# Performance work log

Measured on AMD Instinct MI355X. Metric: run time of the kernel, lower is better.

The kernel has to match this reference:

```python
import jax, jax.numpy as jnp
import numpy as np

B, N, T, D = 64, 76, 128, 128
AH, HEADS, DFF, FAH = 8, 4, 512, 128
DK = D // HEADS


def layer_norm(x, a, b, eps=1e-7):
    mean = x.mean(-1, keepdims=True)
    std = jnp.std(x, -1, ddof=1, keepdims=True)  # torch.std is unbiased
    return a * (x - mean) / (std + eps) + b


def setup_inputs() -> dict:
    key = jax.random.key(0)
    ks = jax.random.split(key, 32)
    w = lambda i, shape, s=0.05: (jax.random.normal(ks[i], shape, jnp.float32) * s)
    return {
        "H": jax.random.normal(ks[0], (B, N, T, D), jnp.float32),
        "mask": jax.random.randint(ks[1], (B, N, T), 0, 2).astype(jnp.float32),
        "feature_mask": jax.random.uniform(ks[2], (B, N), dtype=jnp.float32),
        # MissingAwareTemporalAttention params (shared across features)
        "Wt": w(3, (D, AH), 0.1), "Wx": w(4, (D, AH), 0.1),
        "rate": jnp.array([0.8], jnp.float32),
        "obs_bias": jnp.float32(0.5), "miss_bias": jnp.float32(0.0),
        # MultiHeadedAttention params (weights stored [in,out])
        "Wq": w(5, (D, D)), "bq": jnp.zeros(D, jnp.float32),
        "Wk": w(6, (D, D)), "bk": jnp.zeros(D, jnp.float32),
        "Wv": w(7, (D, D)), "bv": jnp.zeros(D, jnp.float32),
        "Wo": w(8, (D, D)), "bo": jnp.zeros(D, jnp.float32),
        # SublayerConnection LayerNorms
        "ln1_a": jnp.ones(D, jnp.float32), "ln1_b": jnp.zeros(D, jnp.float32),
        "ln2_a": jnp.ones(D, jnp.float32), "ln2_b": jnp.zeros(D, jnp.float32),
        # PositionwiseFeedForward
        "w1": w(9, (D, DFF)), "b1": jnp.zeros(DFF, jnp.float32),
        "w2": w(10, (DFF, D)), "b2": jnp.zeros(D, jnp.float32),
        # FinalAttentionQKV ('mul')
        "fWq": w(11, (D, FAH)), "fbq": jnp.zeros(FAH, jnp.float32),
        "fWk": w(12, (D, FAH)), "fbk": jnp.zeros(FAH, jnp.float32),
        "fWv": w(13, (D, FAH)), "fbv": jnp.zeros(FAH, jnp.float32),
        "mask_scale": jnp.float32(1.0),
    }


def concare_forward(H, mask, feature_mask, Wt, Wx, rate, obs_bias, miss_bias,
                    Wq, bq, Wk, bk, Wv, bv, Wo, bo, ln1_a, ln1_b, ln2_a, ln2_b,
                    w1, b1, w2, b2, fWq, fbq, fWk, fbk, fWv, fbv, mask_scale):
    # ---- MissingAwareTemporalAttention per feature (vectorized over N) ----
    q = jnp.einsum('bnd,da->bna', H[:, :, -1, :], Wt)           # [B,N,AH]
    k = jnp.einsum('bntd,da->bnta', H, Wx)                      # [B,N,T,AH]
    dot = jnp.einsum('bna,bnta->bnt', q, k)                     # [B,N,T]
    b_time = (jnp.arange(T - 1, -1, -1, dtype=jnp.float32) + 1.0)  # [T]
    sig = jax.nn.sigmoid(dot)
    denom = jax.nn.sigmoid(rate[0]) * (jnp.log(2.72 + (1.0 - sig)) * b_time)
    e = jax.nn.relu(sig / denom)
    e = e + jnp.where(mask > 0.5, obs_bias, miss_bias)
    a = jax.nn.softmax(e, axis=-1)                              # over T
    emb = jnp.einsum('bnt,bntd->bnd', a, H)                     # [B,N,D]

    # ---- SublayerConnection 1: pre-norm + MultiHeadedAttention + residual ----
    x0 = layer_norm(emb, ln1_a, ln1_b)
    qh = (x0 @ Wq + bq).reshape(B, N, HEADS, DK).transpose(0, 2, 1, 3)
    kh = (x0 @ Wk + bk).reshape(B, N, HEADS, DK).transpose(0, 2, 1, 3)
    vh = (x0 @ Wv + bv).reshape(B, N, HEADS, DK).transpose(0, 2, 1, 3)
    scores = jnp.einsum('bhqd,bhkd->bhqk', qh, kh) / np.sqrt(DK)
    p = jax.nn.softmax(scores, axis=-1)
    ctx = jnp.einsum('bhqk,bhkd->bhqd', p, vh).transpose(0, 2, 1, 3).reshape(B, N, D)
    mha = ctx @ Wo + bo                                          # [B,N,D]
    # DeCov regularizer over batch, per feature position
    feats = jnp.transpose(mha, (1, 2, 0))                        # [N,D,B]
    centered = feats - feats.mean(axis=2, keepdims=True)
    cov = jnp.einsum('ndb,neb->nde', centered, centered) / (B - 1)
    diag = jnp.einsum('ndd->nd', cov)
    decov = 0.5 * (jnp.sum(cov ** 2) - jnp.sum(diag ** 2))
    x = emb + mha

    # ---- SublayerConnection 2: pre-norm + FFN + residual ----
    x1 = layer_norm(x, ln2_a, ln2_b)
    ffn = jax.nn.relu(x1 @ w1 + b1) @ w2 + b2
    x = x + ffn                                                  # [B,N,D]

    # ---- FinalAttentionQKV ('mul') ----
    fq = x[:, -1, :] @ fWq + fbq                                 # [B,FAH]
    fk = x @ fWk + fbk                                           # [B,N,FAH]
    fv = x @ fWv + fbv                                           # [B,N,FAH]
    fe = jnp.einsum('bna,ba->bn', fk, fq)
    fe = fe + mask_scale * feature_mask
    alpha = jax.nn.softmax(fe, axis=1)                           # over N
    pooled = jnp.einsum('bn,bna->ba', alpha, fv)                 # [B,FAH]
    return pooled, decov


def reference(H, mask, feature_mask, Wt, Wx, rate, obs_bias, miss_bias,
              Wq, bq, Wk, bk, Wv, bv, Wo, bo, ln1_a, ln1_b, ln2_a, ln2_b,
              w1, b1, w2, b2, fWq, fbq, fWk, fbk, fWv, fbv, mask_scale):
    return concare_forward(H, mask, feature_mask, Wt, Wx, rate, obs_bias, miss_bias,
                           Wq, bq, Wk, bk, Wv, bv, Wo, bo, ln1_a, ln1_b, ln2_a, ln2_b,
                           w1, b1, w2, b2, fWq, fbq, fWk, fbk, fWv, fbv, mask_scale)
```

## Files before the change

kernel.cpp:

```cpp
#include <hip/hip_runtime.h>
#include <hip/hip_bf16.h>
#include <math.h>

#define BB 64
#define NN 76
#define TT 128
#define DD 128
#define AH 8
#define NHEADS 4
#define DFF 512
#define FAH 128
#define DK 32
#define BN (BB*NN)
#define ROWS 8
#define NBLK (BN/ROWS)

__global__ __launch_bounds__(512, 6) void k1_temporal(
    const float* __restrict__ H, const float* __restrict__ mask,
    const float* __restrict__ Wt, const float* __restrict__ Wx,
    const float* __restrict__ rate, const float* __restrict__ obs_bias,
    const float* __restrict__ miss_bias, float* __restrict__ emb)
{
    __shared__ __align__(16) float wqs[DD];
    __shared__ __align__(16) float dots[TT];
    __shared__ __align__(16) float as_[TT];
    __shared__ __align__(16) float parts[16][DD];
    __shared__ float qpart[2][AH];
    __shared__ float redmax[2];
    __shared__ float redsum[2];

    const int bid = blockIdx.x;
    const int tid = threadIdx.x;
    const size_t base = (size_t)bid * (TT*DD);

    float r127 = 0.f, maskv = 0.f;
    float4 wt0, wt1, wx0, wx1;
    if (tid < DD) {
        r127 = H[base + (TT-1)*DD + tid];
        wt0 = *(const float4*)&Wt[tid*AH + 0];
        wt1 = *(const float4*)&Wt[tid*AH + 4];
        wx0 = *(const float4*)&Wx[tid*AH + 0];
        wx1 = *(const float4*)&Wx[tid*AH + 4];
        maskv = mask[(size_t)bid*TT + tid];
    }
    const float ratev = rate[0], obsv = obs_bias[0], missv = miss_bias[0];

    float4 h[8];
    const float4* Hg4 = (const float4*)(H + base);
    #pragma unroll
    for (int j = 0; j < 8; ++j) h[j] = Hg4[j*512 + tid];

    if (tid < DD) {
        float p[AH] = {r127*wt0.x, r127*wt0.y, r127*wt0.z, r127*wt0.w,
                       r127*wt1.x, r127*wt1.y, r127*wt1.z, r127*wt1.w};
        #pragma unroll
        for (int a = 0; a < AH; ++a) {
            float v = p[a];
            #pragma unroll
            for (int m = 1; m < 64; m <<= 1) v += __shfl_xor(v, m, 64);
            if ((tid & 63) == 0) qpart[tid >> 6][a] = v;
        }
    }
    __syncthreads();
    if (tid < DD) {
        const float q0 = qpart[0][0]+qpart[1][0], q1 = qpart[0][1]+qpart[1][1];
        const float q2 = qpart[0][2]+qpart[1][2], q3 = qpart[0][3]+qpart[1][3];
        const float q4 = qpart[0][4]+qpart[1][4], q5 = qpart[0][5]+qpart[1][5];
        const float q6 = qpart[0][6]+qpart[1][6], q7 = qpart[0][7]+qpart[1][7];
        wqs[tid] = q0*wx0.x + q1*wx0.y + q2*wx0.z + q3*wx0.w
                 + q4*wx1.x + q5*wx1.y + q6*wx1.z + q7*wx1.w;
    }
    __syncthreads();

    const int c = tid & 31, g = tid >> 5;
    const float4 wq4 = *(const float4*)&wqs[4*c];
    #pragma unroll
    for (int j = 0; j < 8; ++j) {
        float p = h[j].x*wq4.x + h[j].y*wq4.y + h[j].z*wq4.z + h[j].w*wq4.w;
        #pragma unroll
        for (int m = 1; m < 32; m <<= 1) p += __shfl_xor(p, m, 64);
        if (c == 0) dots[g + 16*j] = p;
    }
    __syncthreads();

    const int lane = tid & 63, w = tid >> 6;
    float ev = -1e30f;
    if (tid < TT) {
        const float dot = dots[tid];
        const float sig = 1.f / (1.f + expf(-dot));
        const float sr  = 1.f / (1.f + expf(-ratev));
        const float bt  = (float)(TT - tid);
        const float denom = sr * (logf(2.72f + (1.f - sig)) * bt);
        float e = fmaxf(sig / denom, 0.f);
        e += (maskv > 0.5f) ? obsv : missv;
        ev = e;
        float vmax = ev;
        #pragma unroll
        for (int m = 1; m < 64; m <<= 1) vmax = fmaxf(vmax, __shfl_xor(vmax, m, 64));
        if (lane == 0) redmax[w] = vmax;
    }
    __syncthreads();
    const float mx = fmaxf(redmax[0], redmax[1]);
    const float ex = (tid < TT) ? expf(ev - mx) : 0.f;
    if (tid < TT) {
        float vs = ex;
        #pragma unroll
        for (int m = 1; m < 64; m <<= 1) vs += __shfl_xor(vs, m, 64);
        if (lane == 0) redsum[w] = vs;
    }
    __syncthreads();
    const float ssum = redsum[0] + redsum[1];
    if (tid < TT) as_[tid] = ex / ssum;
    __syncthreads();

    float4 facc = make_float4(0.f, 0.f, 0.f, 0.f);
    #pragma unroll
    for (int j = 0; j < 8; ++j) {
        const float a = as_[g + 16*j];
        facc.x += a*h[j].x; facc.y += a*h[j].y;
        facc.z += a*h[j].z; facc.w += a*h[j].w;
    }
    *(float4*)&parts[g][4*c] = facc;
    __syncthreads();
    if (tid < DD) {
        float acc = 0.f;
        #pragma unroll
        for (int gg = 0; gg < 16; ++gg) acc += parts[gg][tid];
        emb[(size_t)bid*DD + tid] = acc;
    }
}

__global__ __launch_bounds__(256) void k2a_ln_qkv(
    const float* __restrict__ emb,
    const float* __restrict__ ln_a, const float* __restrict__ ln_b,
    const float* __restrict__ Wq, const float* __restrict__ bq,
    const float* __restrict__ Wk, const float* __restrict__ bk,
    const float* __restrict__ Wv, const float* __restrict__ bv,
    float* __restrict__ qb, float* __restrict__ kb, float* __restrict__ vb)
{
    __shared__ float xs[ROWS][DD];
    const int tid = threadIdx.x;
    const int r0 = blockIdx.x * ROWS;

    for (int i = tid; i < ROWS*DD; i += 256) {
        const int r = i / DD, d = i % DD;
        xs[r][d] = emb[(size_t)(r0+r)*DD + d];
    }
    __syncthreads();

    {
        const int wv_ = tid >> 6, lane = tid & 63;
        for (int rr = 0; rr < 2; ++rr) {
            const int r = wv_*2 + rr;
            const float x0 = xs[r][lane], x1 = xs[r][lane+64];
            float s = x0 + x1;
            #pragma unroll
            for (int m = 1; m < 64; m <<= 1) s += __shfl_xor(s, m, 64);
            const float mean = s / (float)DD;
            const float d0 = x0 - mean, d1 = x1 - mean;
            float v = d0*d0 + d1*d1;
            #pragma unroll
            for (int m = 1; m < 64; m <<= 1) v += __shfl_xor(v, m, 64);
            const float inv = 1.f / (sqrtf(v / (float)(DD-1)) + 1e-7f);
            xs[r][lane]    = ln_a[lane]   * (d0*inv) + ln_b[lane];
            xs[r][lane+64] = ln_a[lane+64]* (d1*inv) + ln_b[lane+64];
        }
    }
    __syncthreads();

    const int j = tid & 127, half = tid >> 7, rbase = half*4;
    float aq[4] = {0,0,0,0}, ak[4] = {0,0,0,0}, av[4] = {0,0,0,0};
    for (int d = 0; d < DD; ++d) {
        const float wqv = Wq[d*DD+j], wkv = Wk[d*DD+j], wvv = Wv[d*DD+j];
        #pragma unroll
        for (int r = 0; r < 4; ++r) {
            const float xv = xs[rbase+r][d];
            aq[r] += xv*wqv; ak[r] += xv*wkv; av[r] += xv*wvv;
        }
    }
    const float bqv = bq[j], bkv = bk[j], bvv = bv[j];
    #pragma unroll
    for (int r = 0; r < 4; ++r) {
        const size_t o = (size_t)(r0 + rbase + r)*DD + j;
        qb[o] = aq[r]+bqv; kb[o] = ak[r]+bkv; vb[o] = av[r]+bvv;
    }
}

__global__ __launch_bounds__(128) void k2b_attn(
    const float* __restrict__ qb, const float* __restrict__ kb,
    const float* __restrict__ vb, float* __restrict__ ctx)
{
    __shared__ float Qs[NN][DK], Ks[NN][DK], Vs[NN][DK];
    __shared__ float Ps[NN][NN+1];
    const int b = blockIdx.x / NHEADS, h = blockIdx.x % NHEADS;
    const int tid = threadIdx.x;
    const int co = h*DK;

    for (int i = tid; i < NN*DK; i += 128) {
        const int r = i / DK, c = i % DK;
        const size_t o = (size_t)(b*NN + r)*DD + co + c;
        Qs[r][c] = qb[o]; Ks[r][c] = kb[o]; Vs[r][c] = vb[o];
    }
    __syncthreads();

    const float scale = 0.17677669529663687f;
    if (tid < NN) {
        float qr[DK];
        #pragma unroll
        for (int c = 0; c < DK; ++c) qr[c] = Qs[tid][c];
        float mx = -1e30f;
        for (int k = 0; k < NN; ++k) {
            float s = 0.f;
            #pragma unroll
            for (int c = 0; c < DK; ++c) s += qr[c]*Ks[k][c];
            s *= scale;
            Ps[tid][k] = s;
            mx = fmaxf(mx, s);
        }
        float sum = 0.f;
        for (int k = 0; k < NN; ++k) { const float e = expf(Ps[tid][k]-mx); Ps[tid][k] = e; sum += e; }
        const float inv = 1.f/sum;
        float acc[DK];
        #pragma unroll
        for (int c = 0; c < DK; ++c) acc[c] = 0.f;
        for (int k = 0; k < NN; ++k) {
            const float p = Ps[tid][k];
            #pragma unroll
            for (int c = 0; c < DK; ++c) acc[c] += p*Vs[k][c];
        }
        const size_t o = (size_t)(b*NN + tid)*DD + co;
        #pragma unroll
        for (int c = 0; c < DK; ++c) ctx[o+c] = acc[c]*inv;
    }
}

__global__ __launch_bounds__(256) void k2c_proj_res(
    const float* __restrict__ ctx, const float* __restrict__ emb,
    const float* __restrict__ Wo, const float* __restrict__ bo,
    float* __restrict__ mha, float* __restrict__ x)
{
    __shared__ float cs[ROWS][DD];
    const int tid = threadIdx.x;
    const int r0 = blockIdx.x * ROWS;
    for (int i = tid; i < ROWS*DD; i += 256) {
        const int r = i / DD, d = i % DD;
        cs[r][d] = ctx[(size_t)(r0+r)*DD + d];
    }
    __syncthreads();
    const int j = tid & 127, half = tid >> 7, rbase = half*4;
    float acc[4] = {0,0,0,0};
    for (int d = 0; d < DD; ++d) {
        const float wv = Wo[d*DD+j];
        #pragma unroll
        for (int r = 0; r < 4; ++r) acc[r] += cs[rbase+r][d]*wv;
    }
    const float bov = bo[j];
    #pragma unroll
    for (int r = 0; r < 4; ++r) {
        const size_t o = (size_t)(r0+rbase+r)*DD + j;
        const float m = acc[r] + bov;
        mha[o] = m;
        x[o] = emb[o] + m;
    }
}

__global__ __launch_bounds__(256) void k_decov(
    const float* __restrict__ mha, float* __restrict__ partial)
{
    __shared__ float Cs[BB][DD];
    __shared__ float means[DD];
    __shared__ float reda[256];
    __shared__ float redb[256];
    const int n = blockIdx.x, dc = blockIdx.y;
    const int tid = threadIdx.x;
    for (int i = tid; i < BB*DD; i += 256) {
        const int bb = i / DD, d = i % DD;
        Cs[bb][d] = mha[((size_t)bb*NN + n)*DD + d];
    }
    __syncthreads();
    if (tid < DD) {
        float s = 0.f;
        for (int bb = 0; bb < BB; ++bb) s += Cs[bb][tid];
        means[tid] = s / (float)BB;
    }
    __syncthreads();
    if (tid < DD) {
        const float m = means[tid];
        for (int bb = 0; bb < BB; ++bb) Cs[bb][tid] -= m;
    }
    __syncthreads();
    float ss = 0.f, dd2 = 0.f;
    const float invB1 = 1.f/63.f;
    for (int qi = tid; qi < 1024; qi += 256) {
        const int d  = dc*32 + qi / 32;
        const int e4 = (qi % 32) * 4;
        float a0=0,a1=0,a2=0,a3=0;
        for (int bb = 0; bb < BB; ++bb) {
            const float cd = Cs[bb][d];
            const float4 ce = *(const float4*)&Cs[bb][e4];
            a0 += cd*ce.x; a1 += cd*ce.y; a2 += cd*ce.z; a3 += cd*ce.w;
        }
        a0*=invB1; a1*=invB1; a2*=invB1; a3*=invB1;
        ss += a0*a0+a1*a1+a2*a2+a3*a3;
        if (d >= e4 && d < e4+4) {
            const float c[4] = {a0,a1,a2,a3};
            const float cd = c[d-e4];
            dd2 += cd*cd;
        }
    }
    reda[tid] = ss; redb[tid] = dd2;
    __syncthreads();
    for (int s2 = 128; s2 >= 1; s2 >>= 1) {
        if (tid < s2) { reda[tid] += reda[tid+s2]; redb[tid] += redb[tid+s2]; }
        __syncthreads();
    }
    if (tid == 0) partial[n*4 + dc] = 0.5f*(reda[0] - redb[0]);
}

__global__ __launch_bounds__(256) void k3_ffn(
    const float* __restrict__ x,
    const float* __restrict__ ln_a, const float* __restrict__ ln_b,
    const float* __restrict__ w1, const float* __restrict__ b1,
    const float* __restrict__ w2, const float* __restrict__ b2,
    float* __restrict__ x2)
{
    __shared__ float xs[ROWS][DD];
    __shared__ float x1s[ROWS][DD];
    __shared__ float hs[ROWS][DFF];
    __shared__ float parts[2][ROWS][DD];
    const int tid = threadIdx.x;
    const int r0 = blockIdx.x * ROWS;
    for (int i = tid; i < ROWS*DD; i += 256) {
        const int r = i / DD, d = i % DD;
        xs[r][d] = x[(size_t)(r0+r)*DD + d];
    }
    __syncthreads();
    {
        const int wv_ = tid >> 6, lane = tid & 63;
        for (int rr = 0; rr < 2; ++rr) {
            const int r = wv_*2 + rr;
            const float v0 = xs[r][lane], v1 = xs[r][lane+64];
            float s = v0 + v1;
            #pragma unroll
            for (int m = 1; m < 64; m <<= 1) s += __shfl_xor(s, m, 64);
            const float mean = s / (float)DD;
            const float d0 = v0-mean, d1 = v1-mean;
            float vv = d0*d0 + d1*d1;
            #pragma unroll
            for (int m = 1; m < 64; m <<= 1) vv += __shfl_xor(vv, m, 64);
            const float inv = 1.f / (sqrtf(vv/(float)(DD-1)) + 1e-7f);
            x1s[r][lane]    = ln_a[lane]   * (d0*inv) + ln_b[lane];
            x1s[r][lane+64] = ln_a[lane+64]* (d1*inv) + ln_b[lane+64];
        }
    }
    __syncthreads();
    {
        float acc0[ROWS], acc1[ROWS];
        #pragma unroll
        for (int r = 0; r < ROWS; ++r) { acc0[r]=0.f; acc1[r]=0.f; }
        for (int d = 0; d < DD; ++d) {
            const float wv0 = w1[d*DFF + tid], wv1 = w1[d*DFF + tid + 256];
            #pragma unroll
            for (int r = 0; r < ROWS; ++r) {
                const float xv = x1s[r][d];
                acc0[r] += xv*wv0; acc1[r] += xv*wv1;
            }
        }
        const float b10 = b1[tid], b11 = b1[tid+256];
        #pragma unroll
        for (int r = 0; r < ROWS; ++r) {
            hs[r][tid]     = fmaxf(acc0[r]+b10, 0.f);
            hs[r][tid+256] = fmaxf(acc1[r]+b11, 0.f);
        }
    }
    __syncthreads();
    {
        const int j = tid & 127, half = tid >> 7;
        float acc[ROWS];
        #pragma unroll
        for (int r = 0; r < ROWS; ++r) acc[r] = 0.f;
        for (int k = half*256; k < half*256 + 256; ++k) {
            const float wv = w2[k*DD + j];
            #pragma unroll
            for (int r = 0; r < ROWS; ++r) acc[r] += hs[r][k]*wv;
        }
        #pragma unroll
        for (int r = 0; r < ROWS; ++r) parts[half][r][j] = acc[r];
        __syncthreads();
        if (half == 0) {
            const float b2v = b2[j];
            #pragma unroll
            for (int r = 0; r < ROWS; ++r) {
                const size_t o = (size_t)(r0+r)*DD + j;
                x2[o] = xs[r][j] + parts[0][r][j] + parts[1][r][j] + b2v;
            }
        }
    }
}

__global__ __launch_bounds__(128) void k4_final(
    const float* __restrict__ x, const float* __restrict__ feature_mask,
    const float* __restrict__ fWq, const float* __restrict__ fbq,
    const float* __restrict__ fWk, const float* __restrict__ fbk,
    const float* __restrict__ fWv, const float* __restrict__ fbv,
    const float* __restrict__ mask_scale, const float* __restrict__ decov_partial,
    float* __restrict__ out)
{
    __shared__ float Xs[NN][DD];
    __shared__ float fqs[DD], gs[DD], ys[DD];
    __shared__ float es[NN];
    __shared__ float sc[2];
    const int b = blockIdx.x;
    const int tid = threadIdx.x;
    for (int i = tid; i < NN*DD; i += 128) {
        const int r = i / DD, d = i % DD;
        Xs[r][d] = x[((size_t)b*NN + r)*DD + d];
    }
    __syncthreads();
    {
        float acc = 0.f;
        for (int d = 0; d < DD; ++d) acc += Xs[NN-1][d] * fWq[d*FAH + tid];
        fqs[tid] = acc + fbq[tid];
    }
    __syncthreads();
    {
        float acc = 0.f;
        for (int a = 0; a < FAH; ++a) acc += fWk[tid*FAH + a] * fqs[a];
        gs[tid] = acc;
    }
    if (tid == 0) {
        float acc = 0.f;
        for (int a = 0; a < FAH; ++a) acc += fbk[a]*fqs[a];
        sc[0] = acc;
    }
    __syncthreads();
    const float msc = mask_scale[0];
    if (tid < NN) {
        float acc = 0.f;
        for (int d = 0; d < DD; ++d) acc += Xs[tid][d]*gs[d];
        es[tid] = acc + sc[0] + msc * feature_mask[b*NN + tid];
    }
    __syncthreads();
    if (tid == 0) {
        float mx = -1e30f;
        for (int n2 = 0; n2 < NN; ++n2) mx = fmaxf(mx, es[n2]);
        float sum = 0.f;
        for (int n2 = 0; n2 < NN; ++n2) { const float e = expf(es[n2]-mx); es[n2] = e; sum += e; }
        sc[1] = 1.f/sum;
    }
    __syncthreads();
    {
        const float inv = sc[1];
        float acc = 0.f;
        for (int n2 = 0; n2 < NN; ++n2) acc += es[n2]*Xs[n2][tid];
        ys[tid] = acc * inv;
    }
    __syncthreads();
    {
        float acc = 0.f;
        for (int d = 0; d < DD; ++d) acc += ys[d]*fWv[d*FAH + tid];
        out[(size_t)b*FAH + tid] = acc + fbv[tid];
    }
    if (b == 0 && tid == 0) {
        float s = 0.f;
        for (int i = 0; i < NN*4; ++i) s += decov_partial[i];
        out[BB*FAH] = s;
    }
}

extern "C" void kernel_launch(void* const* d_in, const int* in_sizes, int n_in,
                              void* d_out, int out_size, void* d_ws, size_t ws_size,
                              hipStream_t stream) {
    const float* H    = (const float*)d_in[0];
    const float* mask = (const float*)d_in[1];
    const float* fm   = (const float*)d_in[2];
    const float* Wt   = (const float*)d_in[3];
    const float* Wx   = (const float*)d_in[4];
    const float* rate = (const float*)d_in[5];
    const float* obs_bias  = (const float*)d_in[6];
    const float* miss_bias = (const float*)d_in[7];
    const float* Wq = (const float*)d_in[8];   const float* bq = (const float*)d_in[9];
    const float* Wk = (const float*)d_in[10];  const float* bk = (const float*)d_in[11];
    const float* Wv = (const float*)d_in[12];  const float* bv = (const float*)d_in[13];
    const float* Wo = (const float*)d_in[14];  const float* bo = (const float*)d_in[15];
    const float* ln1a = (const float*)d_in[16]; const float* ln1b = (const float*)d_in[17];
    const float* ln2a = (const float*)d_in[18]; const float* ln2b = (const float*)d_in[19];
    const float* w1 = (const float*)d_in[20];  const float* b1 = (const float*)d_in[21];
    const float* w2 = (const float*)d_in[22];  const float* b2 = (const float*)d_in[23];
    const float* fWq = (const float*)d_in[24]; const float* fbq = (const float*)d_in[25];
    const float* fWk = (const float*)d_in[26]; const float* fbk = (const float*)d_in[27];
    const float* fWv = (const float*)d_in[28]; const float* fbv = (const float*)d_in[29];
    const float* mask_scale = (const float*)d_in[30];
    float* out = (float*)d_out;

    float* ws = (float*)d_ws;
    const size_t S = (size_t)BN*DD;
    float* emb = ws;
    float* qb  = ws + 1*S;
    float* kb  = ws + 2*S;
    float* vb  = ws + 3*S;
    float* ctx = ws + 4*S;
    float* mha = ws + 5*S;
    float* xb  = ws + 6*S;
    float* x2  = ws + 7*S;
    float* dpart = ws + 8*S;

    k1_temporal<<<BN, 512, 0, stream>>>(H, mask, Wt, Wx, rate, obs_bias, miss_bias, emb);
    k2a_ln_qkv<<<NBLK, 256, 0, stream>>>(emb, ln1a, ln1b, Wq, bq, Wk, bk, Wv, bv, qb, kb, vb);
    k2b_attn<<<BB*NHEADS, 128, 0, stream>>>(qb, kb, vb, ctx);
    k2c_proj_res<<<NBLK, 256, 0, stream>>>(ctx, emb, Wo, bo, mha, xb);
    k_decov<<<dim3(NN, 4), 256, 0, stream>>>(mha, dpart);
    k3_ffn<<<NBLK, 256, 0, stream>>>(xb, ln2a, ln2b, w1, b1, w2, b2, x2);
    k4_final<<<BB, 128, 0, stream>>>(x2, fm, fWq, fbq, fWk, fbk, fWv, fbv, mask_scale, dpart, out);
}
```

Baseline: 184.6 us.

## Persistent double-buffered temporal kernel and fuse projection with FFN

The temporal attention kernel becomes persistent with a fixed grid of 512 blocks. Each block loops over (b,n) rows and prefetches the next row's H tile into a second register buffer while it computes the current one, so global load latency overlaps with compute. Separately, the output projection/residual kernel is fused with the LayerNorm+FFN kernel, which removes one launch and the round trip of the intermediate x buffer through global memory. The risks are higher register pressure from the two 8×float4 buffers (launch bounds lowered to 4 blocks per CU) and larger shared memory use in the fused kernel.

```diff
diff --git a/kernel.cpp b/kernel.cpp
--- a/kernel.cpp
+++ b/kernel.cpp
@@ -14,8 +14,9 @@
 #define BN (BB*NN)
 #define ROWS 8
 #define NBLK (BN/ROWS)
-
-__global__ __launch_bounds__(512, 6) void k1_temporal(
+#define K1GRID 512
+
+__global__ __launch_bounds__(512, 4) void k1_temporal(
     const float* __restrict__ H, const float* __restrict__ mask,
     const float* __restrict__ Wt, const float* __restrict__ Wx,
     const float* __restrict__ rate, const float* __restrict__ obs_bias,
@@ -29,104 +30,123 @@
     __shared__ float redmax[2];
     __shared__ float redsum[2];
 
-    const int bid = blockIdx.x;
     const int tid = threadIdx.x;
-    const size_t base = (size_t)bid * (TT*DD);
-
-    float r127 = 0.f, maskv = 0.f;
-    float4 wt0, wt1, wx0, wx1;
+    const int c = tid & 31, g = tid >> 5;
+    const int lane = tid & 63, w = tid >> 6;
+
+    float4 wt0 = {0,0,0,0}, wt1 = {0,0,0,0}, wx0 = {0,0,0,0}, wx1 = {0,0,0,0};
     if (tid < DD) {
-        r127 = H[base + (TT-1)*DD + tid];
         wt0 = *(const float4*)&Wt[tid*AH + 0];
         wt1 = *(const float4*)&Wt[tid*AH + 4];
         wx0 = *(const float4*)&Wx[tid*AH + 0];
         wx1 = *(const float4*)&Wx[tid*AH + 4];
-        maskv = mask[(size_t)bid*TT + tid];
     }
     const float ratev = rate[0], obsv = obs_bias[0], missv = miss_bias[0];
-
-    float4 h[8];
-    const float4* Hg4 = (const float4*)(H + base);
-    #pragma unroll
-    for (int j = 0; j < 8; ++j) h[j] = Hg4[j*512 + tid];
-
-    if (tid < DD) {
-        float p[AH] = {r127*wt0.x, r127*wt0.y, r127*wt0.z, r127*wt0.w,
-                       r127*wt1.x, r127*wt1.y, r127*wt1.z, r127*wt1.w};
-        #pragma unroll
-        for (int a = 0; a < AH; ++a) {
-            float v = p[a];
-            #pragma unroll
-            for (int m = 1; m < 64; m <<= 1) v += __shfl_xor(v, m, 64);
-            if ((tid & 63) == 0) qpart[tid >> 6][a] = v;
-        }
-    }
-    __syncthreads();
-    if (tid < DD) {
-        const float q0 = qpart[0][0]+qpart[1][0], q1 = qpart[0][1]+qpart[1][1];
-        const float q2 = qpart[0][2]+qpart[1][2], q3 = qpart[0][3]+qpart[1][3];
-        const float q4 = qpart[0][4]+qpart[1][4], q5 = qpart[0][5]+qpart[1][5];
-        const float q6 = qpart[0][6]+qpart[1][6], q7 = qpart[0][7]+qpart[1][7];
-        wqs[tid] = q0*wx0.x + q1*wx0.y + q2*wx0.z + q3*wx0.w
-                 + q4*wx1.x + q5*wx1.y + q6*wx1.z + q7*wx1.w;
-    }
-    __syncthreads();
-
-    const int c = tid & 31, g = tid >> 5;
-    const float4 wq4 = *(const float4*)&wqs[4*c];
-    #pragma unroll
-    for (int j = 0; j < 8; ++j) {
-        float p = h[j].x*wq4.x + h[j].y*wq4.y + h[j].z*wq4.z + h[j].w*wq4.w;
-        #pragma unroll
-        for (int m = 1; m < 32; m <<= 1) p += __shfl_xor(p, m, 64);
-        if (c == 0) dots[g + 16*j] = p;
-    }
-    __syncthreads();
-
-    const int lane = tid & 63, w = tid >> 6;
-    float ev = -1e30f;
-    if (tid < TT) {
-        const float dot = dots[tid];
-        const float sig = 1.f / (1.f + expf(-dot));
-        const float sr  = 1.f / (1.f + expf(-ratev));
-        const float bt  = (float)(TT - tid);
-        const float denom = sr * (logf(2.72f + (1.f - sig)) * bt);
-        float e = fmaxf(sig / denom, 0.f);
-        e += (maskv > 0.5f) ? obsv : missv;
-        ev = e;
-        float vmax = ev;
-        #pragma unroll
-        for (int m = 1; m < 64; m <<= 1) vmax = fmaxf(vmax, __shfl_xor(vmax, m, 64));
-        if (lane == 0) redmax[w] = vmax;
-    }
-    __syncthreads();
-    const float mx = fmaxf(redmax[0], redmax[1]);
-    const float ex = (tid < TT) ? expf(ev - mx) : 0.f;
-    if (tid < TT) {
-        float vs = ex;
-        #pragma unroll
-        for (int m = 1; m < 64; m <<= 1) vs += __shfl_xor(vs, m, 64);
-        if (lane == 0) redsum[w] = vs;
-    }
-    __syncthreads();
-    const float ssum = redsum[0] + redsum[1];
-    if (tid < TT) as_[tid] = ex / ssum;
-    __syncthreads();
-
-    float4 facc = make_float4(0.f, 0.f, 0.f, 0.f);
-    #pragma unroll
-    for (int j = 0; j < 8; ++j) {
-        const float a = as_[g + 16*j];
-        facc.x += a*h[j].x; facc.y += a*h[j].y;
-        facc.z += a*h[j].z; facc.w += a*h[j].w;
-    }
-    *(float4*)&parts[g][4*c] = facc;
-    __syncthreads();
-    if (tid < DD) {
-        float acc = 0.f;
-        #pragma unroll
-        for (int gg = 0; gg < 16; ++gg) acc += parts[gg][tid];
-        emb[(size_t)bid*DD + tid] = acc;
+    const float sr = 1.f / (1.f + expf(-ratev));
+
+    auto issue = [&](float4 (&h)[8], float& r127, float& maskv, int t) {
+        const size_t base = (size_t)t * (TT*DD);
+        if (tid < DD) {
+            r127  = H[base + (TT-1)*DD + tid];
+            maskv = mask[(size_t)t*TT + tid];
+        }
+        const float4* Hg4 = (const float4*)(H + base);
+        #pragma unroll
+        for (int j = 0; j < 8; ++j) h[j] = Hg4[j*512 + tid];
+    };
+
+    auto compute = [&](float4 (&h)[8], float r127, float maskv, int t) {
+        if (tid < DD) {
+            float p[AH] = {r127*wt0.x, r127*wt0.y, r127*wt0.z, r127*wt0.w,
+                           r127*wt1.x, r127*wt1.y, r127*wt1.z, r127*wt1.w};
+            #pragma unroll
+            for (int a = 0; a < AH; ++a) {
+                float v = p[a];
+                #pragma unroll
+                for (int m = 1; m < 64; m <<= 1) v += __shfl_xor(v, m, 64);
+                if (lane == 0) qpart[w][a] = v;
+            }
+        }
+        __syncthreads();
+        if (tid < DD) {
+            const float q0 = qpart[0][0]+qpart[1][0], q1 = qpart[0][1]+qpart[1][1];
+            const float q2 = qpart[0][2]+qpart[1][2], q3 = qpart[0][3]+qpart[1][3];
+            const float q4 = qpart[0][4]+qpart[1][4], q5 = qpart[0][5]+qpart[1][5];
+            const float q6 = qpart[0][6]+qpart[1][6], q7 = qpart[0][7]+qpart[1][7];
+            wqs[tid] = q0*wx0.x + q1*wx0.y + q2*wx0.z + q3*wx0.w
+                     + q4*wx1.x + q5*wx1.y + q6*wx1.z + q7*wx1.w;
+        }
+        __syncthreads();
+
+        const float4 wq4 = *(const float4*)&wqs[4*c];
+        #pragma unroll
+        for (int j = 0; j < 8; ++j) {
+            float p = h[j].x*wq4.x + h[j].y*wq4.y + h[j].z*wq4.z + h[j].w*wq4.w;
+            #pragma unroll
+            for (int m = 1; m < 32; m <<= 1) p += __shfl_xor(p, m, 64);
+            if (c == 0) dots[g + 16*j] = p;
+        }
+        __syncthreads();
+
+        float ev = -1e30f;
+        if (tid < TT) {
+            const float dot = dots[tid];
+            const float sig = 1.f / (1.f + expf(-dot));
+            const float bt  = (float)(TT - tid);
+            const float denom = sr * (logf(2.72f + (1.f - sig)) * bt);
+            float e = fmaxf(sig / denom, 0.f);
+            e += (maskv > 0.5f) ? obsv : missv;
+            ev = e;
+            float vmax = ev;
+            #pragma unroll
+            for (int m = 1; m < 64; m <<= 1) vmax = fmaxf(vmax, __shfl_xor(vmax, m, 64));
+            if (lane == 0) redmax[w] = vmax;
+        }
+        __syncthreads();
+        const float mx = fmaxf(redmax[0], redmax[1]);
+        const float ex = (tid < TT) ? expf(ev - mx) : 0.f;
+        if (tid < TT) {
+            float vs = ex;
+            #pragma unroll
+            for (int m = 1; m < 64; m <<= 1) vs += __shfl_xor(vs, m, 64);
+            if (lane == 0) redsum[w] = vs;
+        }
+        __syncthreads();
+        const float ssum = redsum[0] + redsum[1];
+        if (tid < TT) as_[tid] = ex / ssum;
+        __syncthreads();
+
+        float4 facc = make_float4(0.f, 0.f, 0.f, 0.f);
+        #pragma unroll
+        for (int j = 0; j < 8; ++j) {
+            const float a = as_[g + 16*j];
+            facc.x += a*h[j].x; facc.y += a*h[j].y;
+            facc.z += a*h[j].z; facc.w += a*h[j].w;
+        }
+        *(float4*)&parts[g][4*c] = facc;
+        __syncthreads();
+        if (tid < DD) {
+            float acc = 0.f;
+            #pragma unroll
+            for (int gg = 0; gg < 16; ++gg) acc += parts[gg][tid];
+            emb[(size_t)t*DD + tid] = acc;
+        }
+    };
+
+    float4 hA[8], hB[8];
+    float rA = 0.f, rB = 0.f, mA = 0.f, mB = 0.f;
+    int t = blockIdx.x;
+    issue(hA, rA, mA, t);
+    while (true) {
+        const int n1 = t + K1GRID;
+        if (n1 < BN) issue(hB, rB, mB, n1);
+        compute(hA, rA, mA, t);
+        if (n1 >= BN) break;
+        const int n2 = n1 + K1GRID;
+        if (n2 < BN) issue(hA, rA, mA, n2);
+        compute(hB, rB, mB, n1);
+        if (n2 >= BN) break;
+        t = n2;
     }
 }
 
@@ -234,33 +254,109 @@
     }
 }
 
-__global__ __launch_bounds__(256) void k2c_proj_res(
+__global__ __launch_bounds__(256) void k23_proj_ffn(
     const float* __restrict__ ctx, const float* __restrict__ emb,
     const float* __restrict__ Wo, const float* __restrict__ bo,
-    float* __restrict__ mha, float* __restrict__ x)
+    const float* __restrict__ ln_a, const float* __restrict__ ln_b,
+    const float* __restrict__ w1, const float* __restrict__ b1,
+    const float* __restrict__ w2, const float* __restrict__ b2,
+    float* __restrict__ mha, float* __restrict__ x2)
 {
     __shared__ float cs[ROWS][DD];
+    __shared__ float xs[ROWS][DD];
+    __shared__ float x1s[ROWS][DD];
+    __shared__ float hs[ROWS][DFF];
+    __shared__ float parts[2][ROWS][DD];
     const int tid = threadIdx.x;
     const int r0 = blockIdx.x * ROWS;
+
     for (int i = tid; i < ROWS*DD; i += 256) {
         const int r = i / DD, d = i % DD;
         cs[r][d] = ctx[(size_t)(r0+r)*DD + d];
     }
     __syncthreads();
-    const int j = tid & 127, half = tid >> 7, rbase = half*4;
-    float acc[4] = {0,0,0,0};
-    for (int d = 0; d < DD; ++d) {
-        const float wv = Wo[d*DD+j];
-        #pragma unroll
-        for (int r = 0; r < 4; ++r) acc[r] += cs[rbase+r][d]*wv;
-    }
-    const float bov = bo[j];
-    #pragma unroll
-    for (int r = 0; r < 4; ++r) {
-        const size_t o = (size_t)(r0+rbase+r)*DD + j;
-        const float m = acc[r] + bov;
-        mha[o] = m;
-        x[o] = emb[o] + m;
+
+    {
+        const int j = tid & 127, half = tid >> 7, rbase = half*4;
+        float acc[4] = {0,0,0,0};
+        for (int d = 0; d < DD; ++d) {
+            const float wv = Wo[d*DD+j];
+            #pragma unroll
+            for (int r = 0; r < 4; ++r) acc[r] += cs[rbase+r][d]*wv;
+        }
+        const float bov = bo[j];
+        #pragma unroll
+        for (int r = 0; r < 4; ++r) {
+            const size_t o = (size_t)(r0+rbase+r)*DD + j;
+            const float m = acc[r] + bov;
+            mha[o] = m;
+            xs[rbase+r][j] = emb[o] + m;
+        }
+    }
+    __syncthreads();
+
+    {
+        const int wv_ = tid >> 6, lane = tid & 63;
+        for (int rr = 0; rr < 2; ++rr) {
+            const int r = wv_*2 + rr;
+            const float v0 = xs[r][lane], v1 = xs[r][lane+64];
+            float s = v0 + v1;
+            #pragma unroll
+            for (int m = 1; m < 64; m <<= 1) s += __shfl_xor(s, m, 64);
+            const float mean = s / (float)DD;
+            const float d0 = v0-mean, d1 = v1-mean;
+            float vv = d0*d0 + d1*d1;
+            #pragma unroll
+            for (int m = 1; m < 64; m <<= 1) vv += __shfl_xor(vv, m, 64);
+            const float inv = 1.f / (sqrtf(vv/(float)(DD-1)) + 1e-7f);
+            x1s[r][lane]    = ln_a[lane]   * (d0*inv) + ln_b[lane];
+            x1s[r][lane+64] = ln_a[lane+64]* (d1*inv) + ln_b[lane+64];
+        }
+    }
+    __syncthreads();
+
+    {
+        float acc0[ROWS], acc1[ROWS];
+        #pragma unroll
+        for (int r = 0; r < ROWS; ++r) { acc0[r]=0.f; acc1[r]=0.f; }
+        for (int d = 0; d < DD; ++d) {
+            const float wv0 = w1[d*DFF + tid], wv1 = w1[d*DFF + tid + 256];
+            #pragma unroll
+            for (int r = 0; r < ROWS; ++r) {
+                const float xv = x1s[r][d];
+                acc0[r] += xv*wv0; acc1[r] += xv*wv1;
+            }
+        }
+        const float b10 = b1[tid], b11 = b1[tid+256];
+        #pragma unroll
+        for (int r = 0; r < ROWS; ++r) {
+            hs[r][tid]     = fmaxf(acc0[r]+b10, 0.f);
+            hs[r][tid+256] = fmaxf(acc1[r]+b11, 0.f);
+        }
+    }
+    __syncthreads();
+
+    {
+        const int j = tid & 127, half = tid >> 7;
+        float acc[ROWS];
+        #pragma unroll
+        for (int r = 0; r < ROWS; ++r) acc[r] = 0.f;
+        for (int k = half*256; k < half*256 + 256; ++k) {
+            const float wv = w2[k*DD + j];
+            #pragma unroll
+            for (int r = 0; r < ROWS; ++r) acc[r] += hs[r][k]*wv;
+        }
+        #pragma unroll
+        for (int r = 0; r < ROWS; ++r) parts[half][r][j] = acc[r];
+        __syncthreads();
+        if (half == 0) {
+            const float b2v = b2[j];
+            #pragma unroll
+            for (int r = 0; r < ROWS; ++r) {
+                const size_t o = (size_t)(r0+r)*DD + j;
+                x2[o] = xs[r][j] + parts[0][r][j] + parts[1][r][j] + b2v;
+            }
+        }
     }
 }
 
@@ -315,87 +411,6 @@
         __syncthreads();
     }
     if (tid == 0) partial[n*4 + dc] = 0.5f*(reda[0] - redb[0]);
-}
-
-__global__ __launch_bounds__(256) void k3_ffn(
-    const float* __restrict__ x,
-    const float* __restrict__ ln_a, const float* __restrict__ ln_b,
-    const float* __restrict__ w1, const float* __restrict__ b1,
-    const float* __restrict__ w2, const float* __restrict__ b2,
-    float* __restrict__ x2)
-{
-    __shared__ float xs[ROWS][DD];
-    __shared__ float x1s[ROWS][DD];
-    __shared__ float hs[ROWS][DFF];
-    __shared__ float parts[2][ROWS][DD];
-    const int tid = threadIdx.x;
-    const int r0 = blockIdx.x * ROWS;
-    for (int i = tid; i < ROWS*DD; i += 256) {
-        const int r = i / DD, d = i % DD;
-        xs[r][d] = x[(size_t)(r0+r)*DD + d];
-    }
-    __syncthreads();
-    {
-        const int wv_ = tid >> 6, lane = tid & 63;
-        for (int rr = 0; rr < 2; ++rr) {
-            const int r = wv_*2 + rr;
-            const float v0 = xs[r][lane], v1 = xs[r][lane+64];
-            float s = v0 + v1;
-            #pragma unroll
-            for (int m = 1; m < 64; m <<= 1) s += __shfl_xor(s, m, 64);
-            const float mean = s / (float)DD;
-            const float d0 = v0-mean, d1 = v1-mean;
-            float vv = d0*d0 + d1*d1;
-            #pragma unroll
-            for (int m = 1; m < 64; m <<= 1) vv += __shfl_xor(vv, m, 64);
-            const float inv = 1.f / (sqrtf(vv/(float)(DD-1)) + 1e-7f);
-            x1s[r][lane]    = ln_a[lane]   * (d0*inv) + ln_b[lane];
-            x1s[r][lane+64] = ln_a[lane+64]* (d1*inv) + ln_b[lane+64];
-        }
-    }
-    __syncthreads();
-    {
-        float acc0[ROWS], acc1[ROWS];
-        #pragma unroll
-        for (int r = 0; r < ROWS; ++r) { acc0[r]=0.f; acc1[r]=0.f; }
-        for (int d = 0; d < DD; ++d) {
-            const float wv0 = w1[d*DFF + tid], wv1 = w1[d*DFF + tid + 256];
-            #pragma unroll
-            for (int r = 0; r < ROWS; ++r) {
-                const float xv = x1s[r][d];
-                acc0[r] += xv*wv0; acc1[r] += xv*wv1;
-            }
-        }
-        const float b10 = b1[tid], b11 = b1[tid+256];
-        #pragma unroll
-        for (int r = 0; r < ROWS; ++r) {
-            hs[r][tid]     = fmaxf(acc0[r]+b10, 0.f);
-            hs[r][tid+256] = fmaxf(acc1[r]+b11, 0.f);
-        }
-    }
-    __syncthreads();
-    {
-        const int j = tid & 127, half = tid >> 7;
-        float acc[ROWS];
-        #pragma unroll
-        for (int r = 0; r < ROWS; ++r) acc[r] = 0.f;
-        for (int k = half*256; k < half*256 + 256; ++k) {
-            const float wv = w2[k*DD + j];
-            #pragma unroll
-            for (int r = 0; r < ROWS; ++r) acc[r] += hs[r][k]*wv;
-        }
-        #pragma unroll
-        for (int r = 0; r < ROWS; ++r) parts[half][r][j] = acc[r];
-        __syncthreads();
-        if (half == 0) {
-            const float b2v = b2[j];
-            #pragma unroll
-            for (int r = 0; r < ROWS; ++r) {
-                const size_t o = (size_t)(r0+r)*DD + j;
-                x2[o] = xs[r][j] + parts[0][r][j] + parts[1][r][j] + b2v;
-            }
-        }
-    }
 }
 
 __global__ __launch_bounds__(128) void k4_final(
@@ -501,15 +516,13 @@
     float* vb  = ws + 3*S;
     float* ctx = ws + 4*S;
     float* mha = ws + 5*S;
-    float* xb  = ws + 6*S;
-    float* x2  = ws + 7*S;
-    float* dpart = ws + 8*S;
-
-    k1_temporal<<<BN, 512, 0, stream>>>(H, mask, Wt, Wx, rate, obs_bias, miss_bias, emb);
+    float* x2  = ws + 6*S;
+    float* dpart = ws + 7*S;
+
+    k1_temporal<<<K1GRID, 512, 0, stream>>>(H, mask, Wt, Wx, rate, obs_bias, miss_bias, emb);
     k2a_ln_qkv<<<NBLK, 256, 0, stream>>>(emb, ln1a, ln1b, Wq, bq, Wk, bk, Wv, bv, qb, kb, vb);
     k2b_attn<<<BB*NHEADS, 128, 0, stream>>>(qb, kb, vb, ctx);
-    k2c_proj_res<<<NBLK, 256, 0, stream>>>(ctx, emb, Wo, bo, mha, xb);
+    k23_proj_ffn<<<NBLK, 256, 0, stream>>>(ctx, emb, Wo, bo, ln2a, ln2b, w1, b1, w2, b2, mha, x2);
     k_decov<<<dim3(NN, 4), 256, 0, stream>>>(mha, dpart);
-    k3_ffn<<<NBLK, 256, 0, stream>>>(xb, ln2a, ln2b, w1, b1, w2, b2, x2);
     k4_final<<<BB, 128, 0, stream>>>(x2, fm, fWq, fbq, fWk, fbk, fWv, fbv, mask_scale, dpart, out);
 }
```

Result: slower. 216.7 us (+17.4%).
